# Kernel tuning notes

Measured on AMD Instinct MI355X. Metric: run time of the kernel, lower is better.

The kernel has to match this reference:

```python
import jax, jax.numpy as jnp
import numpy as np

N_HEADS = 16
N_EMBD = 1024

def setup_inputs() -> dict:
    key = jax.random.key(0)
    k1, k2, k3, k4, k5 = jax.random.split(key, 5)
    B, T, C = 4, 2048, N_EMBD
    x = jax.random.normal(k1, (B, T, C), dtype=jnp.float32)
    # Linear weights stored as [in, out] (equivalent math to torch's x @ W.T + b)
    W_attn = jax.random.normal(k2, (C, 3 * C), dtype=jnp.float32) * 0.02
    b_attn = jax.random.normal(k3, (3 * C,), dtype=jnp.float32) * 0.02
    W_proj = jax.random.normal(k4, (C, C), dtype=jnp.float32) * 0.02
    b_proj = jax.random.normal(k5, (C,), dtype=jnp.float32) * 0.02
    return {"x": x, "W_attn": W_attn, "b_attn": b_attn, "W_proj": W_proj, "b_proj": b_proj}

def reference(x, W_attn, b_attn, W_proj, b_proj):
    B, T, C = x.shape
    H = N_HEADS
    D = C // H
    scale = 1.0 / jnp.sqrt(jnp.asarray(D, dtype=x.dtype))
    # fused QKV projection
    qkv = x @ W_attn + b_attn                      # [B, T, 3C]
    q, k, v = jnp.split(qkv, 3, axis=-1)           # each [B, T, C]
    q = q.reshape(B, T, H, D)
    k = k.reshape(B, T, H, D)
    v = v.reshape(B, T, H, D)
    # non-causal SDPA
    scores = jnp.einsum('bqhd,bkhd->bhqk', q, k) * scale  # [B, H, T, T]
    attn = jax.nn.softmax(scores, axis=-1)
    y = jnp.einsum('bhqk,bkhd->bqhd', attn, v)     # [B, T, H, D]
    y = y.reshape(B, T, C)
    return y @ W_proj + b_proj
```

## Files before the change

### kernel.cpp

```cpp
#include <hip/hip_runtime.h>

typedef short s16x8 __attribute__((ext_vector_type(8)));
typedef short s16x4 __attribute__((ext_vector_type(4)));
typedef float f32x4 __attribute__((ext_vector_type(4)));

__device__ __forceinline__ unsigned short f2bf(float f) {
  unsigned u = __float_as_uint(f);
  u += 0x7fffu + ((u >> 16) & 1u);
  return (unsigned short)(u >> 16);
}
__device__ __forceinline__ float bf2f(unsigned short h) {
  return __uint_as_float(((unsigned)h) << 16);
}

__device__ __forceinline__ f32x4 mfma16_bf16(s16x4 a, s16x4 b, f32x4 c) {
#if __has_builtin(__builtin_amdgcn_mfma_f32_16x16x16bf16_1k)
  return __builtin_amdgcn_mfma_f32_16x16x16bf16_1k(a, b, c, 0, 0, 0);
#else
  asm volatile("v_mfma_f32_16x16x16_bf16 %0, %1, %2, %0" : "+v"(c) : "v"(a), "v"(b));
  return c;
#endif
}

#define GLOAD_LDS16(g, l)                                          \
  __builtin_amdgcn_global_load_lds(                                \
      (const __attribute__((address_space(1))) void*)(g),          \
      (__attribute__((address_space(3))) void*)(l), 16, 0, 0)


__global__ __launch_bounds__(256) void cvt_x_bf16(const float* __restrict__ in,
                                                  unsigned short* __restrict__ out) {
  int i = (blockIdx.x * 256 + threadIdx.x) * 4;
  float4 v = *(const float4*)(in + i);
  ushort4 o;
  o.x = f2bf(v.x); o.y = f2bf(v.y); o.z = f2bf(v.z); o.w = f2bf(v.w);
  *(ushort4*)(out + i) = o;
}

__global__ __launch_bounds__(256) void transpose_w(const float* __restrict__ W,
                                                   unsigned short* __restrict__ Wt,
                                                   int R, int C) {
  __shared__ float tile[32][33];
  int c0 = blockIdx.x * 32, r0 = blockIdx.y * 32;
  int x = threadIdx.x, ty = threadIdx.y;
  for (int yy = ty; yy < 32; yy += 8)
    tile[yy][x] = W[(size_t)(r0 + yy) * C + c0 + x];
  __syncthreads();
  for (int yy = ty; yy < 32; yy += 8)
    Wt[(size_t)(c0 + yy) * R + r0 + x] = f2bf(tile[x][yy]);
}

__global__ __launch_bounds__(256) void transpose_v(const unsigned short* __restrict__ qkv,
                                                   unsigned short* __restrict__ vt) {
  __shared__ unsigned short TT[32][72];
  const int bh = blockIdx.y;
  const int t0 = blockIdx.x * 32;
  const int b = bh >> 4, h = bh & 15;
  const int t = threadIdx.x;
  {
    int row = t >> 3, c8 = (t & 7) * 8;
    const unsigned short* src =
        qkv + (size_t)(b * 2048 + t0 + row) * 3072 + 2048 + h * 64 + c8;
    *(uint4*)&TT[row][c8] = *(const uint4*)src;
  }
  __syncthreads();
  {
    int drow = t >> 2, tc8 = (t & 3) * 8;
    uint4 val;
    unsigned short* vp = (unsigned short*)&val;
    for (int j = 0; j < 8; j++) vp[j] = TT[tc8 + j][drow];
    *(uint4*)(vt + (size_t)(bh * 64 + drow) * 2048 + t0 + tc8) = val;
  }
}


template <bool OUT_BF16>
__global__ __launch_bounds__(256) void gemm_bt(const unsigned short* __restrict__ A,
                                               const unsigned short* __restrict__ Bt,
                                               const float* __restrict__ bias,
                                               void* __restrict__ Cout,
                                               int M, int N, int K) {
  __shared__ __align__(16) unsigned short As[128 * 32];
  __shared__ __align__(16) unsigned short Bs[128 * 32];

  const int tid  = threadIdx.x;
  const int lane = tid & 63;
  const int w    = tid >> 6;
  const int lr   = lane & 15;
  const int quad = lane >> 4;
  const int wm   = (w >> 1) * 64;
  const int wn   = (w & 1) * 64;
  const int m0   = blockIdx.x * 128;
  const int n0   = blockIdx.y * 128;

  f32x4 acc[4][4];
  for (int i = 0; i < 4; i++)
    for (int j = 0; j < 4; j++)
      acc[i][j] = f32x4{0.f, 0.f, 0.f, 0.f};

  const int srow = tid >> 2;
  const int scb  = (tid & 3) * 8;
  const unsigned short* Ap = A  + (size_t)(m0 + srow) * K + scb;
  const unsigned short* Bp = Bt + (size_t)(n0 + srow) * K + scb;
  unsigned short* lA0 = As + w * 512;
  unsigned short* lA1 = As + 2048 + w * 512;
  unsigned short* lB0 = Bs + w * 512;
  unsigned short* lB1 = Bs + 2048 + w * 512;

  for (int kk = 0; kk < K; kk += 32) {
    __syncthreads();
    GLOAD_LDS16(Ap + kk, lA0);
    GLOAD_LDS16(Ap + (size_t)64 * K + kk, lA1);
    GLOAD_LDS16(Bp + kk, lB0);
    GLOAD_LDS16(Bp + (size_t)64 * K + kk, lB1);
    __syncthreads();

    s16x8 af[4], bf[4];
    for (int i = 0; i < 4; i++) af[i] = *(const s16x8*)&As[(wm + i * 16 + lr) * 32 + quad * 8];
    for (int j = 0; j < 4; j++) bf[j] = *(const s16x8*)&Bs[(wn + j * 16 + lr) * 32 + quad * 8];
    for (int i = 0; i < 4; i++)
      for (int j = 0; j < 4; j++)
        acc[i][j] = __builtin_amdgcn_mfma_f32_16x16x32_bf16(af[i], bf[j], acc[i][j], 0, 0, 0);
  }

  for (int j = 0; j < 4; j++) {
    int col = n0 + wn + j * 16 + lr;
    float bc = bias[col];
    for (int i = 0; i < 4; i++) {
      int rowb = m0 + wm + i * 16 + quad * 4;
      for (int r = 0; r < 4; r++) {
        float v = acc[i][j][r] + bc;
        if (OUT_BF16)
          ((unsigned short*)Cout)[(size_t)(rowb + r) * N + col] = f2bf(v);
        else
          ((float*)Cout)[(size_t)(rowb + r) * N + col] = v;
      }
    }
  }
}


__global__ __launch_bounds__(128, 2) void attn_flash(const unsigned short* __restrict__ qkv,
                                                     const unsigned short* __restrict__ vt,
                                                     unsigned short* __restrict__ y) {
  const int T = 2048, C3 = 3072;
  const int bh = blockIdx.x & 63;
  const int qt = blockIdx.x >> 6;
  const int b  = bh >> 4;
  const int h  = bh & 15;
  const int q0 = qt * 128;

  const int tid  = threadIdx.x;
  const int lane = tid & 63;
  const int w    = tid >> 6;
  const int lr   = lane & 15;
  const int quad = lane >> 4;

  __shared__ __align__(16) unsigned short Ks[64][70];
  __shared__ __align__(16) unsigned short Vs[64][70];

  s16x8 qf[4][2];
  const float QSC = 0.18033688f;
  for (int j = 0; j < 4; j++)
    for (int c = 0; c < 2; c++) {
      const unsigned short* qp =
          qkv + (size_t)(b * T + q0 + w * 64 + j * 16 + lr) * C3 + h * 64 + c * 32 + quad * 8;
      s16x8 t = *(const s16x8*)qp;
      s16x8 o;
      for (int e = 0; e < 8; e++)
        o[e] = (short)f2bf(bf2f((unsigned short)t[e]) * QSC);
      qf[j][c] = o;
    }

  f32x4 O[4][4];
  for (int j = 0; j < 4; j++)
    for (int dt = 0; dt < 4; dt++) O[j][dt] = f32x4{0.f, 0.f, 0.f, 0.f};
  float l[4] = {0.f, 0.f, 0.f, 0.f};

  const int srow = tid >> 3;
  const int sc8  = (tid & 7) * 8;
  const unsigned short* kbase = qkv + (size_t)(b * T) * C3 + 1024 + (size_t)h * 64;
  const unsigned short* vbase = vt + (size_t)(bh * 64) * 2048;

  for (int kt = 0; kt < 32; kt++) {
    const int k0 = kt * 64;
    __syncthreads();
    for (int rr = 0; rr < 64; rr += 16)
      *(uint4*)&Ks[srow + rr][sc8] =
          *(const uint4*)(kbase + (size_t)(k0 + srow + rr) * C3 + sc8);
    for (int rr = 0; rr < 64; rr += 16)
      *(uint4*)&Vs[srow + rr][sc8] =
          *(const uint4*)(vbase + (size_t)(srow + rr) * 2048 + k0 + sc8);
    __syncthreads();

    for (int i = 0; i < 4; i++) {
      s16x8 kf0 = *(const s16x8*)&Ks[i * 16 + lr][quad * 8];
      s16x8 kf1 = *(const s16x8*)&Ks[i * 16 + lr][32 + quad * 8];
      s16x4 vf[4];
      for (int dt = 0; dt < 4; dt++)
        vf[dt] = *(const s16x4*)&Vs[dt * 16 + lr][i * 16 + quad * 4];

      for (int j = 0; j < 4; j++) {
        f32x4 S = f32x4{0.f, 0.f, 0.f, 0.f};
        S = __builtin_amdgcn_mfma_f32_16x16x32_bf16(kf0, qf[j][0], S, 0, 0, 0);
        S = __builtin_amdgcn_mfma_f32_16x16x32_bf16(kf1, qf[j][1], S, 0, 0, 0);
        float p0 = __builtin_amdgcn_exp2f(S[0]);
        float p1 = __builtin_amdgcn_exp2f(S[1]);
        float p2 = __builtin_amdgcn_exp2f(S[2]);
        float p3 = __builtin_amdgcn_exp2f(S[3]);
        l[j] += (p0 + p1) + (p2 + p3);
        s16x4 pa;
        pa[0] = (short)f2bf(p0);
        pa[1] = (short)f2bf(p1);
        pa[2] = (short)f2bf(p2);
        pa[3] = (short)f2bf(p3);
        for (int dt = 0; dt < 4; dt++)
          O[j][dt] = mfma16_bf16(pa, vf[dt], O[j][dt]);
      }
    }
  }

  for (int j = 0; j < 4; j++) {
    float s = l[j];
    s += __shfl_xor(s, 16, 64);
    s += __shfl_xor(s, 32, 64);
    l[j] = 1.f / s;
  }
  for (int j = 0; j < 4; j++) {
    float inv[4];
    for (int r = 0; r < 4; r++) inv[r] = __shfl(l[j], quad * 4 + r, 64);
    for (int dt = 0; dt < 4; dt++) {
      int col = h * 64 + dt * 16 + lr;
      for (int r = 0; r < 4; r++) {
        int row = b * T + q0 + w * 64 + j * 16 + quad * 4 + r;
        y[(size_t)row * 1024 + col] = f2bf(O[j][dt][r] * inv[r]);
      }
    }
  }
}


extern "C" void kernel_launch(void* const* d_in, const int* in_sizes, int n_in,
                              void* d_out, int out_size, void* d_ws, size_t ws_size,
                              hipStream_t stream) {
  const float* x  = (const float*)d_in[0];
  const float* Wa = (const float*)d_in[1];
  const float* ba = (const float*)d_in[2];
  const float* Wp = (const float*)d_in[3];
  const float* bp = (const float*)d_in[4];
  float* out = (float*)d_out;

  char* ws = (char*)d_ws;
  unsigned short* xb  = (unsigned short*)ws;
  unsigned short* Wat = (unsigned short*)(ws + 16777216);
  unsigned short* Wpt = (unsigned short*)(ws + 23068672);
  unsigned short* qkv = (unsigned short*)(ws + 25165824);
  unsigned short* vtr = (unsigned short*)(ws + 75497472);

  cvt_x_bf16<<<8192, 256, 0, stream>>>(x, xb);
  transpose_w<<<dim3(96, 32), dim3(32, 8), 0, stream>>>(Wa, Wat, 1024, 3072);
  transpose_w<<<dim3(32, 32), dim3(32, 8), 0, stream>>>(Wp, Wpt, 1024, 1024);

  gemm_bt<true><<<dim3(64, 24), 256, 0, stream>>>(xb, Wat, ba, qkv, 8192, 3072, 1024);

  transpose_v<<<dim3(64, 64), 256, 0, stream>>>(qkv, vtr);

  attn_flash<<<1024, 128, 0, stream>>>(qkv, vtr, xb);

  gemm_bt<false><<<dim3(64, 8), 256, 0, stream>>>(xb, Wpt, bp, out, 8192, 1024, 1024);
}
```

Measured before the change: 298.7 us.

## Split attention block into 4 waves, swizzle LDS tiles, cheaper bf16 packing

```diff
diff --git a/kernel.cpp b/kernel.cpp
--- a/kernel.cpp
+++ b/kernel.cpp
@@ -140,7 +140,7 @@
 }
 
 
-__global__ __launch_bounds__(128, 2) void attn_flash(const unsigned short* __restrict__ qkv,
+__global__ __launch_bounds__(256, 4) void attn_flash(const unsigned short* __restrict__ qkv,
                                                      const unsigned short* __restrict__ vt,
                                                      unsigned short* __restrict__ y) {
   const int T = 2048, C3 = 3072;
@@ -156,15 +156,15 @@
   const int lr   = lane & 15;
   const int quad = lane >> 4;
 
-  __shared__ __align__(16) unsigned short Ks[64][70];
-  __shared__ __align__(16) unsigned short Vs[64][70];
-
-  s16x8 qf[4][2];
+  __shared__ __align__(16) unsigned short Ks[64][64];
+  __shared__ __align__(16) unsigned short Vs[64][64];
+
+  s16x8 qf[2][2];
   const float QSC = 0.18033688f;
-  for (int j = 0; j < 4; j++)
+  for (int j = 0; j < 2; j++)
     for (int c = 0; c < 2; c++) {
       const unsigned short* qp =
-          qkv + (size_t)(b * T + q0 + w * 64 + j * 16 + lr) * C3 + h * 64 + c * 32 + quad * 8;
+          qkv + (size_t)(b * T + q0 + w * 32 + j * 16 + lr) * C3 + h * 64 + c * 32 + quad * 8;
       s16x8 t = *(const s16x8*)qp;
       s16x8 o;
       for (int e = 0; e < 8; e++)
@@ -172,35 +172,42 @@
       qf[j][c] = o;
     }
 
-  f32x4 O[4][4];
-  for (int j = 0; j < 4; j++)
+  f32x4 O[2][4];
+  for (int j = 0; j < 2; j++)
     for (int dt = 0; dt < 4; dt++) O[j][dt] = f32x4{0.f, 0.f, 0.f, 0.f};
-  float l[4] = {0.f, 0.f, 0.f, 0.f};
+  float l[2] = {0.f, 0.f};
 
   const int srow = tid >> 3;
   const int sc8  = (tid & 7) * 8;
+  const int scb  = sc8 * 2;
   const unsigned short* kbase = qkv + (size_t)(b * T) * C3 + 1024 + (size_t)h * 64;
   const unsigned short* vbase = vt + (size_t)(bh * 64) * 2048;
+  char* KsB = (char*)Ks;
+  char* VsB = (char*)Vs;
+  const int rswz = (lr & 7) << 4;
 
   for (int kt = 0; kt < 32; kt++) {
     const int k0 = kt * 64;
     __syncthreads();
-    for (int rr = 0; rr < 64; rr += 16)
-      *(uint4*)&Ks[srow + rr][sc8] =
-          *(const uint4*)(kbase + (size_t)(k0 + srow + rr) * C3 + sc8);
-    for (int rr = 0; rr < 64; rr += 16)
-      *(uint4*)&Vs[srow + rr][sc8] =
-          *(const uint4*)(vbase + (size_t)(srow + rr) * 2048 + k0 + sc8);
+    for (int rr = 0; rr < 64; rr += 32) {
+      int row = srow + rr;
+      int sw  = scb ^ ((row & 7) << 4);
+      *(uint4*)(KsB + row * 128 + sw) =
+          *(const uint4*)(kbase + (size_t)(k0 + row) * C3 + sc8);
+      *(uint4*)(VsB + row * 128 + sw) =
+          *(const uint4*)(vbase + (size_t)row * 2048 + k0 + sc8);
+    }
     __syncthreads();
 
     for (int i = 0; i < 4; i++) {
-      s16x8 kf0 = *(const s16x8*)&Ks[i * 16 + lr][quad * 8];
-      s16x8 kf1 = *(const s16x8*)&Ks[i * 16 + lr][32 + quad * 8];
+      const char* krow = KsB + (i * 16 + lr) * 128;
+      s16x8 kf0 = *(const s16x8*)(krow + ((quad * 16) ^ rswz));
+      s16x8 kf1 = *(const s16x8*)(krow + ((64 + quad * 16) ^ rswz));
       s16x4 vf[4];
       for (int dt = 0; dt < 4; dt++)
-        vf[dt] = *(const s16x4*)&Vs[dt * 16 + lr][i * 16 + quad * 4];
-
-      for (int j = 0; j < 4; j++) {
+        vf[dt] = *(const s16x4*)(VsB + (dt * 16 + lr) * 128 + ((i * 32 + quad * 8) ^ rswz));
+
+      for (int j = 0; j < 2; j++) {
         f32x4 S = f32x4{0.f, 0.f, 0.f, 0.f};
         S = __builtin_amdgcn_mfma_f32_16x16x32_bf16(kf0, qf[j][0], S, 0, 0, 0);
         S = __builtin_amdgcn_mfma_f32_16x16x32_bf16(kf1, qf[j][1], S, 0, 0, 0);
@@ -209,30 +216,32 @@
         float p2 = __builtin_amdgcn_exp2f(S[2]);
         float p3 = __builtin_amdgcn_exp2f(S[3]);
         l[j] += (p0 + p1) + (p2 + p3);
-        s16x4 pa;
-        pa[0] = (short)f2bf(p0);
-        pa[1] = (short)f2bf(p1);
-        pa[2] = (short)f2bf(p2);
-        pa[3] = (short)f2bf(p3);
+        unsigned u0 = __float_as_uint(p0) + 0x8000u;
+        unsigned u1 = __float_as_uint(p1) + 0x8000u;
+        unsigned u2 = __float_as_uint(p2) + 0x8000u;
+        unsigned u3 = __float_as_uint(p3) + 0x8000u;
+        union { unsigned u[2]; s16x4 v; } pk;
+        pk.u[0] = __builtin_amdgcn_perm(u1, u0, 0x07060302u);
+        pk.u[1] = __builtin_amdgcn_perm(u3, u2, 0x07060302u);
         for (int dt = 0; dt < 4; dt++)
-          O[j][dt] = mfma16_bf16(pa, vf[dt], O[j][dt]);
+          O[j][dt] = mfma16_bf16(pk.v, vf[dt], O[j][dt]);
       }
     }
   }
 
-  for (int j = 0; j < 4; j++) {
+  for (int j = 0; j < 2; j++) {
     float s = l[j];
     s += __shfl_xor(s, 16, 64);
     s += __shfl_xor(s, 32, 64);
     l[j] = 1.f / s;
   }
-  for (int j = 0; j < 4; j++) {
+  for (int j = 0; j < 2; j++) {
     float inv[4];
     for (int r = 0; r < 4; r++) inv[r] = __shfl(l[j], quad * 4 + r, 64);
     for (int dt = 0; dt < 4; dt++) {
       int col = h * 64 + dt * 16 + lr;
       for (int r = 0; r < 4; r++) {
-        int row = b * T + q0 + w * 64 + j * 16 + quad * 4 + r;
+        int row = b * T + q0 + w * 32 + j * 16 + quad * 4 + r;
         y[(size_t)row * 1024 + col] = f2bf(O[j][dt][r] * inv[r]);
       }
     }
@@ -265,7 +274,7 @@
 
   transpose_v<<<dim3(64, 64), 256, 0, stream>>>(qkv, vtr);
 
-  attn_flash<<<1024, 128, 0, stream>>>(qkv, vtr, xb);
+  attn_flash<<<1024, 256, 0, stream>>>(qkv, vtr, xb);
 
   gemm_bt<false><<<dim3(64, 8), 256, 0, stream>>>(xb, Wpt, bp, out, 8192, 1024, 1024);
 }
```

Result: faster. 291.6 us (-2.4%).
